# Kernel optimization log

Hardware: AMD Instinct MI355X
Metric: run time of the kernel (lower is better)

Reference implementation:

```python
import jax, jax.numpy as jnp
import numpy as np


def setup_inputs() -> dict:
    key = jax.random.key(0)
    k1, k2 = jax.random.split(key)
    B, L, C, H, W = 1, 16, 8, 128, 128
    # flows scaled so cumulative displacements stay mostly inside [-1, 1]
    flows = jax.random.normal(k1, (B, L, 2, H, W), jnp.float32) * 0.1
    images = jax.random.normal(k2, (B, L, C, H, W), jnp.float32)
    return {"flows": flows, "images": images}


def _base_grid(H, W, dtype):
    step_y, step_x = 2.0 / H, 2.0 / W
    gy = jnp.linspace(-1.0 + step_y * 0.5, 1.0 - step_y * 0.5, H, dtype=dtype)
    gx = jnp.linspace(-1.0 + step_x * 0.5, 1.0 - step_x * 0.5, W, dtype=dtype)
    mx, my = jnp.meshgrid(gx, gy, indexing="xy")  # each [H, W]
    return jnp.stack([mx, my], axis=-1)  # [H, W, 2], (x, y)


def _grid_sample_bilinear(img, grid):
    # img: [C, H, W]; grid: [H, W, 2] normalized coords in [-1, 1]
    # matches torch grid_sample(mode='bilinear', padding_mode='zeros', align_corners=False)
    C, H, W = img.shape
    ix = (grid[..., 0] + 1.0) * (W * 0.5) - 0.5
    iy = (grid[..., 1] + 1.0) * (H * 0.5) - 0.5
    x0 = jnp.floor(ix)
    y0 = jnp.floor(iy)
    wx = ix - x0
    wy = iy - y0

    def gather(xf, yf):
        xi = xf.astype(jnp.int32)
        yi = yf.astype(jnp.int32)
        valid = ((xf >= 0) & (xf < W) & (yf >= 0) & (yf < H)).astype(img.dtype)
        xi = jnp.clip(xi, 0, W - 1)
        yi = jnp.clip(yi, 0, H - 1)
        return img[:, yi, xi] * valid  # [C, H, W]

    return (
        gather(x0, y0) * ((1.0 - wx) * (1.0 - wy))
        + gather(x0 + 1.0, y0) * (wx * (1.0 - wy))
        + gather(x0, y0 + 1.0) * ((1.0 - wx) * wy)
        + gather(x0 + 1.0, y0 + 1.0) * (wx * wy)
    )


def reference(flows, images):
    B, L, C, H, W = images.shape
    dtype = flows.dtype
    cum = jnp.cumsum(flows.astype(jnp.float32), axis=1).astype(dtype)  # [B,L,2,H,W]
    base = _base_grid(H, W, dtype)  # [H,W,2]

    # pairwise relative flow: rel[b,t,k] = cum[b,t] - cum[b,k]  -> [B,L,L,2,H,W]
    rel = cum[:, :, None] - cum[:, None, :]
    grid = base + jnp.transpose(rel, (0, 1, 2, 4, 5, 3))  # [B,L,L,H,W,2]
    gx = jnp.remainder(grid[..., 0] + 1.0, 2.0) - 1.0  # wrap x periodically
    grid = jnp.concatenate([gx[..., None], grid[..., 1:]], axis=-1)

    # sample images[b,k] at grid[b,t,k]
    sample_k = jax.vmap(_grid_sample_bilinear, in_axes=(0, 0))       # over k
    sample_tk = jax.vmap(sample_k, in_axes=(None, 0))                # over t
    sample_btk = jax.vmap(sample_tk, in_axes=(0, 0))                 # over b
    sampled = sample_btk(images, grid)  # [B,L,L,C,H,W]

    # triangular accumulation: out[b,t] = sum_{k<=t} sampled[b,t,k]
    mask = jnp.tril(jnp.ones((L, L), dtype=dtype))
    return jnp.einsum("btkchw,tk->btchw", sampled, mask)
```

## Files before the change

kernel.cpp:

```cpp
#include <hip/hip_runtime.h>
#include <hip/hip_fp16.h>

constexpr int L = 16, C = 8, H = 128, W = 128;
constexpr int HW = H * W;

__global__ __launch_bounds__(256) void prep_k(const float* __restrict__ flows,
                                              const float* __restrict__ images,
                                              float* __restrict__ cum,
                                              __half* __restrict__ timg) {
    int b = blockIdx.x;
    constexpr int TB = (L * HW) / 256;
    if (b < TB) {
        int idx = b * 256 + threadIdx.x;
        int l = idx >> 14, pix = idx & (HW - 1);
        const float* src = images + (size_t)l * C * HW + pix;
        float4 packed;
        __half2* hp = reinterpret_cast<__half2*>(&packed);
        hp[0] = __floats2half2_rn(src[0 * HW], src[1 * HW]);
        hp[1] = __floats2half2_rn(src[2 * HW], src[3 * HW]);
        hp[2] = __floats2half2_rn(src[4 * HW], src[5 * HW]);
        hp[3] = __floats2half2_rn(src[6 * HW], src[7 * HW]);
        reinterpret_cast<float4*>(timg)[idx] = packed;
    } else {
        int idx = (b - TB) * 256 + threadIdx.x;
        int comp = idx >> 14, pix = idx & (HW - 1);
        const float* src = flows + comp * HW + pix;
        float* dst = cum + comp * HW + pix;
        float s = 0.f;
#pragma unroll
        for (int l = 0; l < L; ++l) {
            s += src[(size_t)l * 2 * HW];
            dst[(size_t)l * 2 * HW] = s;
        }
    }
}

__device__ __forceinline__ void samp(float acc[8], float relx, float rely,
                                     float bx1, float by1,
                                     const __half* __restrict__ img) {
    float xr = bx1 + relx;
    xr = fmaf(-2.0f, floorf(xr * 0.5f), xr);
    float yr = by1 + rely;
    float ix = xr * (W * 0.5f) - 0.5f;
    float iy = yr * (H * 0.5f) - 0.5f;
    float x0f = floorf(ix), y0f = floorf(iy);
    float wx = ix - x0f, wy = iy - y0f;
#pragma unroll
    for (int dy = 0; dy < 2; ++dy) {
#pragma unroll
        for (int dx = 0; dx < 2; ++dx) {
            float xf = x0f + (float)dx;
            float yf = y0f + (float)dy;
            bool valid = (xf >= 0.f) & (xf < (float)W) & (yf >= 0.f) & (yf < (float)H);
            float wgt = (dx ? wx : 1.f - wx) * (dy ? wy : 1.f - wy);
            wgt = valid ? wgt : 0.f;
            int xi = (int)xf; xi = xi < 0 ? 0 : (xi > W - 1 ? W - 1 : xi);
            int yi = (int)yf; yi = yi < 0 ? 0 : (yi > H - 1 ? H - 1 : yi);
            float4 raw = *reinterpret_cast<const float4*>(img + (yi * W + xi) * C);
            const __half* hv = reinterpret_cast<const __half*>(&raw);
#pragma unroll
            for (int c = 0; c < 8; ++c)
                acc[c] = fmaf(__half2float(hv[c]), wgt, acc[c]);
        }
    }
}

constexpr int TPB = 128;
__global__ __launch_bounds__(TPB) void sample_k(const float* __restrict__ cum,
                                                const __half* __restrict__ timg,
                                                float* __restrict__ out) {
    int p   = blockIdx.x >> 7;
    int pix = (blockIdx.x & 127) * TPB + threadIdx.x;
    int h = pix >> 7, w = pix & (W - 1);
    float bx1 = (w + 0.5f) * (2.0f / W);
    float by1 = (h + 0.5f) * (2.0f / H);

    int t1 = p, t2 = 15 - p;
    float c1x = cum[(size_t)(2 * t1)     * HW + pix];
    float c1y = cum[(size_t)(2 * t1 + 1) * HW + pix];
    float c2x = cum[(size_t)(2 * t2)     * HW + pix];
    float c2y = cum[(size_t)(2 * t2 + 1) * HW + pix];

    float acc1[8] = {0, 0, 0, 0, 0, 0, 0, 0};
    float acc2[8] = {0, 0, 0, 0, 0, 0, 0, 0};

    for (int k = 0; k <= t2; ++k) {
        float ckx = cum[(size_t)(2 * k)     * HW + pix];
        float cky = cum[(size_t)(2 * k + 1) * HW + pix];
        const __half* img = timg + (size_t)k * HW * C;
        samp(acc2, c2x - ckx, c2y - cky, bx1, by1, img);
        if (k <= t1)
            samp(acc1, c1x - ckx, c1y - cky, bx1, by1, img);
    }

    size_t o1 = (size_t)t1 * C * HW + pix;
    size_t o2 = (size_t)t2 * C * HW + pix;
#pragma unroll
    for (int c = 0; c < 8; ++c) {
        out[o1 + c * HW] = acc1[c];
        out[o2 + c * HW] = acc2[c];
    }
}

extern "C" void kernel_launch(void* const* d_in, const int* in_sizes, int n_in,
                              void* d_out, int out_size, void* d_ws, size_t ws_size,
                              hipStream_t stream) {
    const float* flows  = (const float*)d_in[0];
    const float* images = (const float*)d_in[1];
    float* out = (float*)d_out;

    float*  cum  = (float*)d_ws;
    __half* timg = (__half*)((char*)d_ws + (size_t)2 * L * HW * sizeof(float));

    prep_k<<<(L * HW) / 256 + (2 * HW) / 256, 256, 0, stream>>>(flows, images, cum, timg);
    sample_k<<<8 * (HW / TPB), TPB, 0, stream>>>(cum, timg, out);
}
```

Measured before the change: 85.58 us.

## Split sampling work into balanced chunks with partial sums and fixup kernel

Instead of pairing time steps t and 15-t in one thread, each block now handles one (t, k-range) chunk. Time steps 8..15 have their k range split in two halves that write partial sums to workspace, and a new fixup kernel adds them into the output. The bilinear sampler is restructured to compute separable edge-masked weights and issue all four texel loads up front. Block size moves from 128 to 256 threads. In exchange the change adds an extra kernel launch, extra global traffic for the partial buffers, and some load imbalance, since chunks range from 1 to 8 samples.

```diff
diff --git a/kernel.cpp b/kernel.cpp
--- a/kernel.cpp
+++ b/kernel.cpp
@@ -3,6 +3,7 @@
 
 constexpr int L = 16, C = 8, H = 128, W = 128;
 constexpr int HW = H * W;
+constexpr int CHW = C * HW;
 
 __global__ __launch_bounds__(256) void prep_k(const float* __restrict__ flows,
                                               const float* __restrict__ images,
@@ -13,7 +14,7 @@
     if (b < TB) {
         int idx = b * 256 + threadIdx.x;
         int l = idx >> 14, pix = idx & (HW - 1);
-        const float* src = images + (size_t)l * C * HW + pix;
+        const float* src = images + (size_t)l * CHW + pix;
         float4 packed;
         __half2* hp = reinterpret_cast<__half2*>(&packed);
         hp[0] = __floats2half2_rn(src[0 * HW], src[1 * HW]);
@@ -41,65 +42,88 @@
     float xr = bx1 + relx;
     xr = fmaf(-2.0f, floorf(xr * 0.5f), xr);
     float yr = by1 + rely;
-    float ix = xr * (W * 0.5f) - 0.5f;
-    float iy = yr * (H * 0.5f) - 0.5f;
+    float ix = fmaf(xr, W * 0.5f, -0.5f);
+    float iy = fmaf(yr, H * 0.5f, -0.5f);
     float x0f = floorf(ix), y0f = floorf(iy);
     float wx = ix - x0f, wy = iy - y0f;
+    int x0 = (int)x0f, y0 = (int)y0f;
+
+    float wx0 = ((unsigned)x0       < (unsigned)W) ? 1.f - wx : 0.f;
+    float wx1 = ((unsigned)(x0 + 1) < (unsigned)W) ? wx       : 0.f;
+    float wy0 = ((unsigned)y0       < (unsigned)H) ? 1.f - wy : 0.f;
+    float wy1 = ((unsigned)(y0 + 1) < (unsigned)H) ? wy       : 0.f;
+    int xi0 = min(max(x0, 0), W - 1), xi1 = min(max(x0 + 1, 0), W - 1);
+    int yi0 = min(max(y0, 0), H - 1), yi1 = min(max(y0 + 1, 0), H - 1);
+
+    const float4* p = reinterpret_cast<const float4*>(img);
+    float4 r00 = p[yi0 * W + xi0];
+    float4 r01 = p[yi0 * W + xi1];
+    float4 r10 = p[yi1 * W + xi0];
+    float4 r11 = p[yi1 * W + xi1];
+    float w00 = wx0 * wy0, w01 = wx1 * wy0, w10 = wx0 * wy1, w11 = wx1 * wy1;
+    const __half* h00 = reinterpret_cast<const __half*>(&r00);
+    const __half* h01 = reinterpret_cast<const __half*>(&r01);
+    const __half* h10 = reinterpret_cast<const __half*>(&r10);
+    const __half* h11 = reinterpret_cast<const __half*>(&r11);
 #pragma unroll
-    for (int dy = 0; dy < 2; ++dy) {
-#pragma unroll
-        for (int dx = 0; dx < 2; ++dx) {
-            float xf = x0f + (float)dx;
-            float yf = y0f + (float)dy;
-            bool valid = (xf >= 0.f) & (xf < (float)W) & (yf >= 0.f) & (yf < (float)H);
-            float wgt = (dx ? wx : 1.f - wx) * (dy ? wy : 1.f - wy);
-            wgt = valid ? wgt : 0.f;
-            int xi = (int)xf; xi = xi < 0 ? 0 : (xi > W - 1 ? W - 1 : xi);
-            int yi = (int)yf; yi = yi < 0 ? 0 : (yi > H - 1 ? H - 1 : yi);
-            float4 raw = *reinterpret_cast<const float4*>(img + (yi * W + xi) * C);
-            const __half* hv = reinterpret_cast<const __half*>(&raw);
-#pragma unroll
-            for (int c = 0; c < 8; ++c)
-                acc[c] = fmaf(__half2float(hv[c]), wgt, acc[c]);
-        }
+    for (int c = 0; c < 8; ++c) {
+        float v = fmaf(__half2float(h00[c]), w00,
+                  fmaf(__half2float(h01[c]), w01,
+                  fmaf(__half2float(h10[c]), w10,
+                       __half2float(h11[c]) * w11)));
+        acc[c] += v;
     }
 }
 
-constexpr int TPB = 128;
-__global__ __launch_bounds__(TPB) void sample_k(const float* __restrict__ cum,
+__global__ __launch_bounds__(256) void sample_k(const float* __restrict__ cum,
                                                 const __half* __restrict__ timg,
-                                                float* __restrict__ out) {
-    int p   = blockIdx.x >> 7;
-    int pix = (blockIdx.x & 127) * TPB + threadIdx.x;
+                                                float* __restrict__ out,
+                                                float* __restrict__ part) {
+    int cid  = blockIdx.x >> 6;
+    int pix  = (blockIdx.x & 63) * 256 + threadIdx.x;
     int h = pix >> 7, w = pix & (W - 1);
     float bx1 = (w + 0.5f) * (2.0f / W);
     float by1 = (h + 0.5f) * (2.0f / H);
 
-    int t1 = p, t2 = 15 - p;
-    float c1x = cum[(size_t)(2 * t1)     * HW + pix];
-    float c1y = cum[(size_t)(2 * t1 + 1) * HW + pix];
-    float c2x = cum[(size_t)(2 * t2)     * HW + pix];
-    float c2y = cum[(size_t)(2 * t2 + 1) * HW + pix];
-
-    float acc1[8] = {0, 0, 0, 0, 0, 0, 0, 0};
-    float acc2[8] = {0, 0, 0, 0, 0, 0, 0, 0};
-
-    for (int k = 0; k <= t2; ++k) {
-        float ckx = cum[(size_t)(2 * k)     * HW + pix];
-        float cky = cum[(size_t)(2 * k + 1) * HW + pix];
-        const __half* img = timg + (size_t)k * HW * C;
-        samp(acc2, c2x - ckx, c2y - cky, bx1, by1, img);
-        if (k <= t1)
-            samp(acc1, c1x - ckx, c1y - cky, bx1, by1, img);
+    int t, k0, k1;
+    float* dst;
+    if (cid < 8) {
+        t = cid; k0 = 0; k1 = t + 1;
+        dst = out + (size_t)t * CHW;
+    } else {
+        int i = (cid - 8) >> 1, odd = (cid - 8) & 1;
+        t = 8 + i;
+        k0 = odd ? 8 : 0;
+        k1 = odd ? t + 1 : 8;
+        dst = part + (size_t)(cid - 8) * CHW;
     }
 
-    size_t o1 = (size_t)t1 * C * HW + pix;
-    size_t o2 = (size_t)t2 * C * HW + pix;
+    float ctx = cum[(size_t)(2 * t)     * HW + pix];
+    float cty = cum[(size_t)(2 * t + 1) * HW + pix];
+
+    float acc[8] = {0, 0, 0, 0, 0, 0, 0, 0};
+    for (int k = k0; k < k1; ++k) {
+        float relx = ctx - cum[(size_t)(2 * k)     * HW + pix];
+        float rely = cty - cum[(size_t)(2 * k + 1) * HW + pix];
+        samp(acc, relx, rely, bx1, by1, timg + (size_t)k * HW * C);
+    }
+
 #pragma unroll
-    for (int c = 0; c < 8; ++c) {
-        out[o1 + c * HW] = acc1[c];
-        out[o2 + c * HW] = acc2[c];
-    }
+    for (int c = 0; c < 8; ++c)
+        dst[(size_t)c * HW + pix] = acc[c];
+}
+
+__global__ __launch_bounds__(256) void fixup_k(const float* __restrict__ part,
+                                               float* __restrict__ out) {
+    int idx = blockIdx.x * 256 + threadIdx.x;
+    constexpr int Q = CHW / 4;
+    int i = idx >> 15, r = idx & (Q - 1);
+    const float4* P = reinterpret_cast<const float4*>(part);
+    float4* O = reinterpret_cast<float4*>(out);
+    float4 a = P[(size_t)(2 * i) * Q + r];
+    float4 b = P[(size_t)(2 * i + 1) * Q + r];
+    O[(size_t)(8 + i) * Q + r] =
+        make_float4(a.x + b.x, a.y + b.y, a.z + b.z, a.w + b.w);
 }
 
 extern "C" void kernel_launch(void* const* d_in, const int* in_sizes, int n_in,
@@ -110,8 +134,10 @@
     float* out = (float*)d_out;
 
     float*  cum  = (float*)d_ws;
-    __half* timg = (__half*)((char*)d_ws + (size_t)2 * L * HW * sizeof(float));
+    __half* timg = (__half*)((char*)d_ws + (size_t)2 * L * HW * 4);
+    float*  part = (float*)((char*)d_ws + (size_t)6 * 1024 * 1024);
 
     prep_k<<<(L * HW) / 256 + (2 * HW) / 256, 256, 0, stream>>>(flows, images, cum, timg);
-    sample_k<<<8 * (HW / TPB), TPB, 0, stream>>>(cum, timg, out);
+    sample_k<<<24 * 64, 256, 0, stream>>>(cum, timg, out, part);
+    fixup_k<<<(8 * CHW / 4) / 256, 256, 0, stream>>>(part, out);
 }
```

New measurement: 89.55 us. +4.6%, slower.
